# Kernel tuning notes

Hardware: AMD Instinct MI355X
Metric: run time of the kernel (lower is better)

Reference implementation:

```python
import jax, jax.numpy as jnp
import numpy as np

D_MODEL = 1024
H = 16           # num_heads
D = 64           # head_dim
HD = H * D       # hd_dim
PHASE_SCALE = 10.0


def _freqs():
    # Multiscale phasor frequencies (H, D): rotary-style per-dim decay,
    # per-head linear scale (reconstruction of generate_multiscale_phasors).
    d = jnp.arange(D, dtype=jnp.float32)
    base = 10000.0 ** (-d / D)                                  # (D,)
    head_scale = (jnp.arange(H, dtype=jnp.float32) + 1.0) / H   # (H,)
    return 2.0 * np.pi * head_scale[:, None] * base[None, :]    # (H, D)


def setup_inputs() -> dict:
    key = jax.random.key(0)
    ks = jax.random.split(key, 4)
    B, T = 2, 8192
    s = 1.0 / np.sqrt(D_MODEL)
    return {
        "x": jax.random.normal(ks[0], (B, T, D_MODEL), jnp.float32),
        "Wk": jax.random.normal(ks[1], (HD, D_MODEL), jnp.float32) * s,
        "Wv": jax.random.normal(ks[2], (HD, D_MODEL), jnp.float32) * s,
        "Wo": jax.random.normal(ks[3], (D_MODEL, HD), jnp.float32) * s,
        "gate": jnp.ones((H, 2), jnp.float32) * 0.5,
    }


def reference(x, Wk, Wv, Wo, gate):
    B, T, C = x.shape
    k_real = (x @ Wk.T).reshape(B, T, H, D)                      # (B,T,H,D)
    v = (x @ Wv.T).reshape(B, T, H, D).astype(jnp.complex64)
    # shared q/k unit-modulus phasors
    k = jnp.exp(1j * (k_real * PHASE_SCALE))                     # complex64
    q = k
    t = jnp.arange(T, dtype=jnp.float32)
    rotors = jnp.exp(1j * (t[:, None, None] * _freqs()[None]))   # (T,H,D)
    scale = jnp.sqrt(jnp.arange(1, T + 1, dtype=jnp.float32))[None, :, None, None]
    # positional path: bind with rotors, accumulate, retrieve with conj rotors
    mem_pos = jnp.cumsum(v * rotors[None], axis=1)
    out_pos = (mem_pos * jnp.conj(rotors)[None]).real / scale
    # associative path: bind with conj of shifted keys, retrieve with q
    k_shifted = jnp.roll(k, shift=1, axis=1).at[:, 0].set(0)
    mem_assoc = jnp.cumsum(v * jnp.conj(k_shifted), axis=1)
    out_assoc = (mem_assoc * q).real / scale
    # gated combine per head
    out = out_pos * gate[None, None, :, 0:1] + out_assoc * gate[None, None, :, 1:2]
    out = out.reshape(B, T, HD)
    return out @ Wo.T
```

## Files before the change

### kernel.cpp

```cpp
#include <hip/hip_runtime.h>
#include <math.h>


#define B_SZ 2
#define T_LEN 8192
#define H_N 16
#define D_N 64
#define HD 1024
#define DM 1024

#define NCH 128
#define CH (T_LEN / NCH)

typedef unsigned short u16;
typedef __attribute__((ext_vector_type(4))) unsigned short u16x4;
typedef __attribute__((ext_vector_type(8))) short s16x8;
typedef __attribute__((ext_vector_type(8))) _Float16 f16x8;
typedef __attribute__((ext_vector_type(4))) float f32x4;

__device__ __forceinline__ u16 f2h(float f) {
    return __builtin_bit_cast(u16, (_Float16)f);
}
__device__ __forceinline__ float h2f(u16 h) {
    return (float)__builtin_bit_cast(_Float16, h);
}

__global__ __launch_bounds__(256) void conv_x_h(
    const float* __restrict__ x, u16* __restrict__ xh)
{
    size_t i = ((size_t)blockIdx.x * 256 + threadIdx.x) * 4;
    float4 v = *reinterpret_cast<const float4*>(&x[i]);
    u16x4 o = { f2h(v.x), f2h(v.y), f2h(v.z), f2h(v.w) };
    *reinterpret_cast<u16x4*>(&xh[i]) = o;
}

__global__ __launch_bounds__(256) void conv_wkv(
    const float* __restrict__ Wk, const float* __restrict__ Wv,
    u16* __restrict__ Wkv)
{
    size_t i = ((size_t)blockIdx.x * 256 + threadIdx.x) * 4;
    int r = (int)(i >> 10);
    size_t src = (i & (1024 * 1024 - 1));
    float4 v;
    float s;
    if (r < 1024) { v = *reinterpret_cast<const float4*>(&Wk[i]); s = 10.f; }
    else          { v = *reinterpret_cast<const float4*>(&Wv[src]); s = 1.f; }
    u16x4 o = { f2h(s * v.x), f2h(s * v.y), f2h(s * v.z), f2h(s * v.w) };
    *reinterpret_cast<u16x4*>(&Wkv[i]) = o;
}

__global__ __launch_bounds__(256) void conv_w(
    const float* __restrict__ W, u16* __restrict__ Wb)
{
    size_t i = ((size_t)blockIdx.x * 256 + threadIdx.x) * 4;
    float4 v = *reinterpret_cast<const float4*>(&W[i]);
    u16x4 o = { f2h(v.x), f2h(v.y), f2h(v.z), f2h(v.w) };
    *reinterpret_cast<u16x4*>(&Wb[i]) = o;
}

#define GBK 64

#define BAR()     asm volatile("s_barrier" ::: "memory")
#define VMCNT4()  asm volatile("s_waitcnt vmcnt(4)" ::: "memory")
#define VMCNT0()  asm volatile("s_waitcnt vmcnt(0)" ::: "memory")
#define LGKM8PRE() asm volatile("s_waitcnt lgkmcnt(8)" ::: "memory")
#define LGKM0_SB() do { asm volatile("s_waitcnt lgkmcnt(0)" ::: "memory"); \
                        __builtin_amdgcn_sched_barrier(0); } while (0)

template <int IMM>
__device__ __forceinline__ s16x8 dsr(unsigned base) {
    s16x8 r;
    asm volatile("ds_read_b128 %0, %1 offset:%2"
                 : "=v"(r) : "v"(base), "n"(IMM));
    return r;
}

__device__ __forceinline__ unsigned lds_addr(const void* p) {
    return (unsigned)(uintptr_t)(const __attribute__((address_space(3))) void*)p;
}

#define MFMA_Q(mh, nh)                                               \
  {                                                                  \
    _Pragma("unroll")                                                \
    for (int ks_ = 0; ks_ < 2; ++ks_)                                \
      _Pragma("unroll")                                              \
      for (int m_ = 0; m_ < 4; ++m_)                                 \
        _Pragma("unroll")                                            \
        for (int n_ = 0; n_ < 2; ++n_)                               \
          acc[(mh)*4 + m_][(nh)*2 + n_] =                            \
            __builtin_amdgcn_mfma_f32_16x16x32_f16(                  \
              __builtin_bit_cast(f16x8, aR[m_][ks_]),                \
              __builtin_bit_cast(f16x8, bR[(nh)*2 + n_][ks_]),       \
              acc[(mh)*4 + m_][(nh)*2 + n_], 0, 0, 0);               \
  }

#define RD_A(ph, ofs)                                                          \
  aR[0][0]=dsr<(ofs)+0>(bA[ph][0]);    aR[1][0]=dsr<(ofs)+2048>(bA[ph][0]);    \
  aR[2][0]=dsr<(ofs)+4096>(bA[ph][0]); aR[3][0]=dsr<(ofs)+6144>(bA[ph][0]);    \
  aR[0][1]=dsr<(ofs)+0>(bA[ph][1]);    aR[1][1]=dsr<(ofs)+2048>(bA[ph][1]);    \
  aR[2][1]=dsr<(ofs)+4096>(bA[ph][1]); aR[3][1]=dsr<(ofs)+6144>(bA[ph][1]);
#define RD_B01(ph)                                                             \
  bR[0][0]=dsr<0>(bB[ph][0]);    bR[1][0]=dsr<2048>(bB[ph][0]);                \
  bR[0][1]=dsr<0>(bB[ph][1]);    bR[1][1]=dsr<2048>(bB[ph][1]);
#define RD_B23(ph)                                                             \
  bR[2][0]=dsr<4096>(bB[ph][0]); bR[3][0]=dsr<6144>(bB[ph][0]);                \
  bR[2][1]=dsr<4096>(bB[ph][1]); bR[3][1]=dsr<6144>(bB[ph][1]);

#define PHASE_GROUP(ph)                                              \
  {                                                                  \
    RD_A(ph, 0); RD_B01(ph); RD_B23(ph);                             \
    LGKM8PRE();                                                      \
    if ((ph) == 0)    { STAGE_A(2*t+1, 1, 0); STAGE_A(2*t+1, 1, 1); }\
    else if (gm)      { STAGE_A(2*t+2, 0, 0); STAGE_A(2*t+2, 0, 1); }\
    BAR(); LGKM0_SB();                                               \
    __builtin_amdgcn_s_setprio(1);                                   \
    MFMA_Q(0, 0); MFMA_Q(0, 1);                                      \
    __builtin_amdgcn_s_setprio(0);                                   \
    BAR();                                                           \
    RD_A(ph, 8192);                                                  \
    if (gm) { STAGE_B(2*t+2+(ph), (ph), 0);                          \
              STAGE_B(2*t+2+(ph), (ph), 1); VMCNT4(); }              \
    else    { VMCNT0(); }                                            \
    BAR(); LGKM0_SB();                                               \
    __builtin_amdgcn_s_setprio(1);                                   \
    MFMA_Q(1, 0); MFMA_Q(1, 1);                                      \
    __builtin_amdgcn_s_setprio(0);                                   \
    BAR();                                                           \
  }

__device__ __forceinline__ void stage_half(
    const u16* __restrict__ g, int ld, int rowbase, int kbase,
    char* ldshalf, int wid, int lane)
{
#pragma unroll
    for (int s = 0; s < 2; ++s) {
        const int slot = s * 512 + wid * 64 + lane;
        const int r = slot >> 3;
        const int cb = ((slot & 7) << 4) ^ ((r & 7) << 4);
        const u16* gp = g + (size_t)(rowbase + r) * ld + kbase + (cb >> 1);
        __builtin_amdgcn_global_load_lds(
            (const __attribute__((address_space(1))) void*)gp,
            (__attribute__((address_space(3))) void*)(ldshalf + s * 8192 + wid * 1024),
            16, 0, 0);
    }
}

__global__ __launch_bounds__(512, 2) void gemm_mfma256(
    const u16* __restrict__ A, int lda, const u16* __restrict__ W, int ldw,
    void* __restrict__ Cv, int ldc, void* __restrict__ Vv, int K, int mode,
    int m_base, int bshift)
{
    __shared__ __align__(16) char lds[131072];

    const int tid  = threadIdx.x;
    const int lane = tid & 63;
    const int wid  = tid >> 6;
    const int wm   = wid >> 2;
    const int wn   = wid & 3;
    const int l15  = lane & 15;
    const int hib  = (lane >> 4) << 4;

    const int flat = blockIdx.y * gridDim.x + blockIdx.x;
    const int xcd  = flat & 7;
    const int c    = flat >> 3;
    const int byl  = c & ((1 << bshift) - 1);
    const int bx   = c >> bshift;
    const int m0   = ((xcd << bshift) + byl) * 256 + m_base;
    const int n0   = bx * 256;

    const int NK2 = K / (2 * GBK);

    f32x4 acc[8][4] = {};
    s16x8 aR[4][2], bR[4][2];

    const int Xl = (l15 & 7) << 4;
    unsigned bA[2][2], bB[2][2];
#pragma unroll
    for (int p2 = 0; p2 < 2; ++p2)
#pragma unroll
        for (int ks = 0; ks < 2; ++ks) {
            bA[p2][ks] = lds_addr(lds) + p2 * 65536 +
                         (wm * 128 + l15) * 128 + ((ks * 64 + hib) ^ Xl);
            bB[p2][ks] = lds_addr(lds) + p2 * 65536 + 32768 +
                         (wn * 64 + l15) * 128 + ((ks * 64 + hib) ^ Xl);
        }

    auto STAGE_A = [&](int kt, int buf, int h) {
        stage_half(A, lda, m0 + h * 128, kt * GBK,
                   (char*)lds + buf * 65536 + h * 16384, wid, lane);
    };
    auto STAGE_B = [&](int kt, int buf, int h) {
        stage_half(W, ldw, n0 + h * 128, kt * GBK,
                   (char*)lds + buf * 65536 + 32768 + h * 16384, wid, lane);
    };

    STAGE_B(0, 0, 0); STAGE_B(0, 0, 1);
    STAGE_A(0, 0, 0); STAGE_A(0, 0, 1);
    STAGE_B(1, 1, 0); STAGE_B(1, 1, 1);
    VMCNT4();
    BAR();

    for (int t = 0; t < NK2; ++t) {
        const bool gm = (t < NK2 - 1);
        PHASE_GROUP(0)
        PHASE_GROUP(1)
    }

    float* Cf = (float*)Cv;
    u16*   Vh = (u16*)Vv;
    const bool isPhase = (mode == 0) || (n0 < 1024);
#pragma unroll
    for (int m = 0; m < 8; ++m) {
#pragma unroll
        for (int n = 0; n < 4; ++n) {
            const int r0  = m0 + wm * 128 + m * 16 + ((lane >> 4) << 2);
            const int col = n0 + wn * 64 + n * 16 + l15;
#pragma unroll
            for (int r = 0; r < 4; ++r) {
                const float val = acc[m][n][r];
                if (isPhase) {
                    Cf[(size_t)(r0 + r) * ldc + col] = val;
                } else {
                    Vh[(size_t)(r0 + r) * 1024 + (col - 1024)] = f2h(val);
                }
            }
        }
    }
}

__device__ __forceinline__ void rotor_sincos(int t, double fd, float* sr, float* cr)
{
    const double twopi = 6.283185307179586;
    const double inv2pi = 0.15915494309189535;
    double ang = (double)t * fd;
    double n = rint(ang * inv2pi);
    float red = (float)(ang - n * twopi);
    __sincosf(red, sr, cr);
}

__global__ __launch_bounds__(256) void scan_pass1(
    const u16* __restrict__ vArr, const float* __restrict__ phase,
    float* __restrict__ cs)
{
    int gw = (blockIdx.x * 256 + threadIdx.x) >> 6;
    int d = threadIdx.x & 63;
    int c = gw & (NCH - 1);
    int h = (gw >> 7) & (H_N - 1);
    int b = gw >> 11;

    double fd = 6.283185307179586 * ((double)(h + 1) / 16.0)
              * pow(10000.0, -(double)d / 64.0);

    int t0 = c * CH;
    size_t base = ((size_t)b * T_LEN + t0) * HD + (size_t)h * D_N + d;

    float cr, sr;
    rotor_sincos(t0, fd, &sr, &cr);
    float cf, sf;
    sincosf((float)fd, &sf, &cf);

    float cp = 0.f, spv = 0.f;
    if (t0 > 0) {
        float thp = phase[base - HD];
        __sincosf(thp, &spv, &cp);
    }

    float sp_re = 0.f, sp_im = 0.f, sa_re = 0.f, sa_im = 0.f;
    for (int i = 0; i < CH; ++i) {
        size_t idx = base + (size_t)i * HD;
        float v = h2f(vArr[idx]);
        float th = phase[idx];
        sp_re = fmaf(v, cr, sp_re);
        sp_im = fmaf(v, sr, sp_im);
        sa_re = fmaf(v, cp, sa_re);
        sa_im = fmaf(-v, spv, sa_im);
        __sincosf(th, &spv, &cp);
        float nc = fmaf(cr, cf, -sr * sf);
        float ns = fmaf(sr, cf,  cr * sf);
        cr = nc; sr = ns;
    }

    const size_t NT = (size_t)B_SZ * H_N * NCH * D_N;
    size_t ci = (size_t)gw * D_N + d;
    cs[ci] = sp_re;
    cs[NT + ci] = sp_im;
    cs[2 * NT + ci] = sa_re;
    cs[3 * NT + ci] = sa_im;
}

__global__ void scan_pass2(float* __restrict__ cs)
{
    int tid = blockIdx.x * blockDim.x + threadIdx.x;
    if (tid >= B_SZ * H_N * D_N) return;
    int d = tid & 63;
    int bh = tid >> 6;
    size_t base = (size_t)bh * NCH * D_N + d;
    const size_t NT = (size_t)B_SZ * H_N * NCH * D_N;
    float r0 = 0.f, r1 = 0.f, r2 = 0.f, r3 = 0.f;
    for (int c = 0; c < NCH; ++c) {
        size_t i = base + (size_t)c * D_N;
        float a = cs[i], b2 = cs[NT + i], c2 = cs[2 * NT + i], d2 = cs[3 * NT + i];
        cs[i] = r0; cs[NT + i] = r1; cs[2 * NT + i] = r2; cs[3 * NT + i] = r3;
        r0 += a; r1 += b2; r2 += c2; r3 += d2;
    }
}

__global__ __launch_bounds__(256) void scan_pass3(
    const u16* __restrict__ vArr, const float* __restrict__ phase,
    const float* __restrict__ cs, const float* __restrict__ gate,
    u16* __restrict__ y)
{
    int gw = (blockIdx.x * 256 + threadIdx.x) >> 6;
    int d = threadIdx.x & 63;
    int c = gw & (NCH - 1);
    int h = (gw >> 7) & (H_N - 1);
    int b = gw >> 11;

    double fd = 6.283185307179586 * ((double)(h + 1) / 16.0)
              * pow(10000.0, -(double)d / 64.0);
    float g0 = gate[h * 2 + 0];
    float g1 = gate[h * 2 + 1];

    int t0 = c * CH;
    size_t base = ((size_t)b * T_LEN + t0) * HD + (size_t)h * D_N + d;

    const size_t NT = (size_t)B_SZ * H_N * NCH * D_N;
    size_t ci = (size_t)gw * D_N + d;
    float ap_re = cs[ci];
    float ap_im = cs[NT + ci];
    float aa_re = cs[2 * NT + ci];
    float aa_im = cs[3 * NT + ci];

    float cr, sr;
    rotor_sincos(t0, fd, &sr, &cr);
    float cf, sf;
    sincosf((float)fd, &sf, &cf);

    float cp = 0.f, spv = 0.f;
    if (t0 > 0) {
        float thp = phase[base - HD];
        __sincosf(thp, &spv, &cp);
    }

    for (int i = 0; i < CH; ++i) {
        int t = t0 + i;
        size_t idx = base + (size_t)i * HD;
        float v = h2f(vArr[idx]);
        float th = phase[idx];
        ap_re = fmaf(v, cr, ap_re);
        ap_im = fmaf(v, sr, ap_im);
        aa_re = fmaf(v, cp, aa_re);
        aa_im = fmaf(-v, spv, aa_im);
        float op = fmaf(ap_re, cr, ap_im * sr);
        float ck, sk;
        __sincosf(th, &sk, &ck);
        float oa = fmaf(aa_re, ck, -aa_im * sk);
        float sc = rsqrtf((float)(t + 1));
        y[idx] = f2h((g0 * op + g1 * oa) * sc);
        cp = ck; spv = sk;
        float nc = fmaf(cr, cf, -sr * sf);
        float ns = fmaf(sr, cf,  cr * sf);
        cr = nc; sr = ns;
    }
}

extern "C" void kernel_launch(void* const* d_in, const int* in_sizes, int n_in,
                              void* d_out, int out_size, void* d_ws, size_t ws_size,
                              hipStream_t stream)
{
    const float* x    = (const float*)d_in[0];
    const float* Wk   = (const float*)d_in[1];
    const float* Wv   = (const float*)d_in[2];
    const float* Wo   = (const float*)d_in[3];
    const float* gate = (const float*)d_in[4];
    float* out = (float*)d_out;

    float* phase = (float*)d_out;

    char* wsb = (char*)d_ws;
    u16*   xh  = (u16*)wsb;
    u16*   yb  = (u16*)wsb;
    u16*   vb  = (u16*)(wsb + (32ull << 20));
    float* cs  = (float*)(wsb + (64ull << 20));
    u16*   Wkv = (u16*)(wsb + (68ull << 20));
    u16*   Wob = (u16*)(wsb + (72ull << 20));

    hipLaunchKernelGGL(conv_x_h, dim3(16384), dim3(256), 0, stream, x, xh);
    hipLaunchKernelGGL(conv_wkv, dim3(2048), dim3(256), 0, stream, Wk, Wv, Wkv);
    hipLaunchKernelGGL(conv_w,   dim3(1024), dim3(256), 0, stream, Wo, Wob);

    const dim3 gblk(512);

    hipLaunchKernelGGL(gemm_mfma256, dim3(8, 32), gblk, 0, stream,
                       xh, 1024, Wkv, 1024, (void*)phase, HD, (void*)vb, 1024, 3,
                       0, 2);
    hipLaunchKernelGGL(gemm_mfma256, dim3(8, 32), gblk, 0, stream,
                       xh, 1024, Wkv, 1024, (void*)phase, HD, (void*)vb, 1024, 3,
                       8192, 2);

    const int waves = B_SZ * H_N * NCH;
    hipLaunchKernelGGL(scan_pass1, dim3(waves / 4), dim3(256), 0, stream, vb, phase, cs);
    hipLaunchKernelGGL(scan_pass2, dim3(8), dim3(256), 0, stream, cs);
    hipLaunchKernelGGL(scan_pass3, dim3(waves / 4), dim3(256), 0, stream, vb, phase, cs, gate, yb);

    hipLaunchKernelGGL(gemm_mfma256, dim3(4, 64), gblk, 0, stream,
                       yb, 1024, Wob, 1024, (void*)out, HD, (void*)0, 1024, 0,
                       0, 3);
}
```

Measured before the change: 186.7 us.

## Restructure GEMM main loop to full-tile double buffering and store phases as fp16

The GEMM main loop is rewritten from a split half-tile staging schedule into one where each K tile issues all A/B global-to-LDS loads for the next tile up front. The LDS register reads are split into A0/A1/B0/B1 groups so MFMAs can start after partial lgkmcnt waits, and there is one vmcnt(0) plus barrier per tile. Separately, the phase output of the K projection is range-reduced modulo 2π and stored as fp16 in a workspace buffer instead of fp32 in the output buffer. This halves the phase traffic read by both scan passes. The fp16 phase storage loses precision on the angle, and the per-tile barrier may reduce overlap compared with the previous schedule.

Measured after the change: 234.8 us. 25.8% more time.

```diff
diff --git a/kernel.cpp b/kernel.cpp
--- a/kernel.cpp
+++ b/kernel.cpp
@@ -61,9 +61,9 @@
 #define GBK 64
 
 #define BAR()     asm volatile("s_barrier" ::: "memory")
-#define VMCNT4()  asm volatile("s_waitcnt vmcnt(4)" ::: "memory")
 #define VMCNT0()  asm volatile("s_waitcnt vmcnt(0)" ::: "memory")
-#define LGKM8PRE() asm volatile("s_waitcnt lgkmcnt(8)" ::: "memory")
+#define LGKM8_SB() do { asm volatile("s_waitcnt lgkmcnt(8)" ::: "memory"); \
+                        __builtin_amdgcn_sched_barrier(0); } while (0)
 #define LGKM0_SB() do { asm volatile("s_waitcnt lgkmcnt(0)" ::: "memory"); \
                         __builtin_amdgcn_sched_barrier(0); } while (0)
 
@@ -79,7 +79,7 @@
     return (unsigned)(uintptr_t)(const __attribute__((address_space(3))) void*)p;
 }
 
-#define MFMA_Q(mh, nh)                                               \
+#define MFMA_Q2(AS, BS, mh, nh)                                      \
   {                                                                  \
     _Pragma("unroll")                                                \
     for (int ks_ = 0; ks_ < 2; ++ks_)                                \
@@ -89,42 +89,50 @@
         for (int n_ = 0; n_ < 2; ++n_)                               \
           acc[(mh)*4 + m_][(nh)*2 + n_] =                            \
             __builtin_amdgcn_mfma_f32_16x16x32_f16(                  \
-              __builtin_bit_cast(f16x8, aR[m_][ks_]),                \
-              __builtin_bit_cast(f16x8, bR[(nh)*2 + n_][ks_]),       \
+              __builtin_bit_cast(f16x8, AS[m_][ks_]),                \
+              __builtin_bit_cast(f16x8, BS[n_][ks_]),                \
               acc[(mh)*4 + m_][(nh)*2 + n_], 0, 0, 0);               \
   }
 
-#define RD_A(ph, ofs)                                                          \
-  aR[0][0]=dsr<(ofs)+0>(bA[ph][0]);    aR[1][0]=dsr<(ofs)+2048>(bA[ph][0]);    \
-  aR[2][0]=dsr<(ofs)+4096>(bA[ph][0]); aR[3][0]=dsr<(ofs)+6144>(bA[ph][0]);    \
-  aR[0][1]=dsr<(ofs)+0>(bA[ph][1]);    aR[1][1]=dsr<(ofs)+2048>(bA[ph][1]);    \
-  aR[2][1]=dsr<(ofs)+4096>(bA[ph][1]); aR[3][1]=dsr<(ofs)+6144>(bA[ph][1]);
-#define RD_B01(ph)                                                             \
-  bR[0][0]=dsr<0>(bB[ph][0]);    bR[1][0]=dsr<2048>(bB[ph][0]);                \
-  bR[0][1]=dsr<0>(bB[ph][1]);    bR[1][1]=dsr<2048>(bB[ph][1]);
-#define RD_B23(ph)                                                             \
-  bR[2][0]=dsr<4096>(bB[ph][0]); bR[3][0]=dsr<6144>(bB[ph][0]);                \
-  bR[2][1]=dsr<4096>(bB[ph][1]); bR[3][1]=dsr<6144>(bB[ph][1]);
-
-#define PHASE_GROUP(ph)                                              \
+#define RD_A0(ph)                                                              \
+  A0r[0][0]=dsr<0>(bA[ph][0]);    A0r[1][0]=dsr<2048>(bA[ph][0]);              \
+  A0r[2][0]=dsr<4096>(bA[ph][0]); A0r[3][0]=dsr<6144>(bA[ph][0]);              \
+  A0r[0][1]=dsr<0>(bA[ph][1]);    A0r[1][1]=dsr<2048>(bA[ph][1]);              \
+  A0r[2][1]=dsr<4096>(bA[ph][1]); A0r[3][1]=dsr<6144>(bA[ph][1]);
+#define RD_A1(ph)                                                              \
+  A1r[0][0]=dsr<8192+0>(bA[ph][0]);    A1r[1][0]=dsr<8192+2048>(bA[ph][0]);    \
+  A1r[2][0]=dsr<8192+4096>(bA[ph][0]); A1r[3][0]=dsr<8192+6144>(bA[ph][0]);    \
+  A1r[0][1]=dsr<8192+0>(bA[ph][1]);    A1r[1][1]=dsr<8192+2048>(bA[ph][1]);    \
+  A1r[2][1]=dsr<8192+4096>(bA[ph][1]); A1r[3][1]=dsr<8192+6144>(bA[ph][1]);
+#define RD_B0(ph)                                                              \
+  B0r[0][0]=dsr<0>(bB[ph][0]);    B0r[1][0]=dsr<2048>(bB[ph][0]);              \
+  B0r[0][1]=dsr<0>(bB[ph][1]);    B0r[1][1]=dsr<2048>(bB[ph][1]);
+#define RD_B1(ph)                                                              \
+  B1r[0][0]=dsr<4096>(bB[ph][0]); B1r[1][0]=dsr<6144>(bB[ph][0]);              \
+  B1r[0][1]=dsr<4096>(bB[ph][1]); B1r[1][1]=dsr<6144>(bB[ph][1]);
+
+#define TILE(ph, kt)                                                 \
   {                                                                  \
-    RD_A(ph, 0); RD_B01(ph); RD_B23(ph);                             \
-    LGKM8PRE();                                                      \
-    if ((ph) == 0)    { STAGE_A(2*t+1, 1, 0); STAGE_A(2*t+1, 1, 1); }\
-    else if (gm)      { STAGE_A(2*t+2, 0, 0); STAGE_A(2*t+2, 0, 1); }\
-    BAR(); LGKM0_SB();                                               \
+    const bool gm = (kt) < NK - 1;                                   \
+    RD_A0(ph); RD_B0(ph);                                            \
+    if (gm) { STAGE_A((kt)+1, (ph)^1, 0); STAGE_A((kt)+1, (ph)^1, 1);\
+              STAGE_B((kt)+1, (ph)^1, 0); STAGE_B((kt)+1, (ph)^1, 1);}\
+    LGKM0_SB();                                     \
+    RD_B1(ph); RD_A1(ph);                          \
+    __builtin_amdgcn_sched_barrier(0);                               \
     __builtin_amdgcn_s_setprio(1);                                   \
-    MFMA_Q(0, 0); MFMA_Q(0, 1);                                      \
+    MFMA_Q2(A0r, B0r, 0, 0);                                         \
     __builtin_amdgcn_s_setprio(0);                                   \
-    BAR();                                                           \
-    RD_A(ph, 8192);                                                  \
-    if (gm) { STAGE_B(2*t+2+(ph), (ph), 0);                          \
-              STAGE_B(2*t+2+(ph), (ph), 1); VMCNT4(); }              \
-    else    { VMCNT0(); }                                            \
-    BAR(); LGKM0_SB();                                               \
+    LGKM8_SB();                             \
     __builtin_amdgcn_s_setprio(1);                                   \
-    MFMA_Q(1, 0); MFMA_Q(1, 1);                                      \
+    MFMA_Q2(A0r, B1r, 0, 1);                                         \
     __builtin_amdgcn_s_setprio(0);                                   \
+    LGKM0_SB();                                        \
+    __builtin_amdgcn_s_setprio(1);                                   \
+    MFMA_Q2(A1r, B0r, 1, 0);                                         \
+    MFMA_Q2(A1r, B1r, 1, 1);                                         \
+    __builtin_amdgcn_s_setprio(0);                                   \
+    VMCNT0();                            \
     BAR();                                                           \
   }
 
@@ -145,7 +153,7 @@
     }
 }
 
-__global__ __launch_bounds__(512, 2) void gemm_mfma256(
+__global__ __launch_bounds__(512, 2) void gemm2p(
     const u16* __restrict__ A, int lda, const u16* __restrict__ W, int ldw,
     void* __restrict__ Cv, int ldc, void* __restrict__ Vv, int K, int mode,
     int m_base, int bshift)
@@ -168,10 +176,10 @@
     const int m0   = ((xcd << bshift) + byl) * 256 + m_base;
     const int n0   = bx * 256;
 
-    const int NK2 = K / (2 * GBK);
+    const int NK = K / GBK;
 
     f32x4 acc[8][4] = {};
-    s16x8 aR[4][2], bR[4][2];
+    s16x8 A0r[4][2], A1r[4][2], B0r[2][2], B1r[2][2];
 
     const int Xl = (l15 & 7) << 4;
     unsigned bA[2][2], bB[2][2];
@@ -194,21 +202,22 @@
                    (char*)lds + buf * 65536 + 32768 + h * 16384, wid, lane);
     };
 
+    STAGE_A(0, 0, 0); STAGE_A(0, 0, 1);
     STAGE_B(0, 0, 0); STAGE_B(0, 0, 1);
-    STAGE_A(0, 0, 0); STAGE_A(0, 0, 1);
-    STAGE_B(1, 1, 0); STAGE_B(1, 1, 1);
-    VMCNT4();
+    VMCNT0();
     BAR();
 
-    for (int t = 0; t < NK2; ++t) {
-        const bool gm = (t < NK2 - 1);
-        PHASE_GROUP(0)
-        PHASE_GROUP(1)
-    }
-
+    for (int t2 = 0; t2 < NK / 2; ++t2) {
+        TILE(0, 2 * t2)
+        TILE(1, 2 * t2 + 1)
+    }
+
+    const float TWOPI  = 6.2831853071795864f;
+    const float INV2PI = 0.15915494309189535f;
     float* Cf = (float*)Cv;
+    u16*   Ph = (u16*)Cv;
     u16*   Vh = (u16*)Vv;
-    const bool isPhase = (mode == 0) || (n0 < 1024);
+    const bool isPhase = (n0 < 1024);
 #pragma unroll
     for (int m = 0; m < 8; ++m) {
 #pragma unroll
@@ -218,8 +227,11 @@
 #pragma unroll
             for (int r = 0; r < 4; ++r) {
                 const float val = acc[m][n][r];
-                if (isPhase) {
+                if (mode == 0) {
                     Cf[(size_t)(r0 + r) * ldc + col] = val;
+                } else if (isPhase) {
+                    float red = fmaf(-TWOPI, rintf(val * INV2PI), val);
+                    Ph[(size_t)(r0 + r) * 1024 + col] = f2h(red);
                 } else {
                     Vh[(size_t)(r0 + r) * 1024 + (col - 1024)] = f2h(val);
                 }
@@ -239,7 +251,7 @@
 }
 
 __global__ __launch_bounds__(256) void scan_pass1(
-    const u16* __restrict__ vArr, const float* __restrict__ phase,
+    const u16* __restrict__ vArr, const u16* __restrict__ phase,
     float* __restrict__ cs)
 {
     int gw = (blockIdx.x * 256 + threadIdx.x) >> 6;
@@ -261,7 +273,7 @@
 
     float cp = 0.f, spv = 0.f;
     if (t0 > 0) {
-        float thp = phase[base - HD];
+        float thp = h2f(phase[base - HD]);
         __sincosf(thp, &spv, &cp);
     }
 
@@ -269,7 +281,7 @@
     for (int i = 0; i < CH; ++i) {
         size_t idx = base + (size_t)i * HD;
         float v = h2f(vArr[idx]);
-        float th = phase[idx];
+        float th = h2f(phase[idx]);
         sp_re = fmaf(v, cr, sp_re);
         sp_im = fmaf(v, sr, sp_im);
         sa_re = fmaf(v, cp, sa_re);
@@ -306,7 +318,7 @@
 }
 
 __global__ __launch_bounds__(256) void scan_pass3(
-    const u16* __restrict__ vArr, const float* __restrict__ phase,
+    const u16* __restrict__ vArr, const u16* __restrict__ phase,
     const float* __restrict__ cs, const float* __restrict__ gate,
     u16* __restrict__ y)
 {
@@ -338,7 +350,7 @@
 
     float cp = 0.f, spv = 0.f;
     if (t0 > 0) {
-        float thp = phase[base - HD];
+        float thp = h2f(phase[base - HD]);
         __sincosf(thp, &spv, &cp);
     }
 
@@ -346,7 +358,7 @@
         int t = t0 + i;
         size_t idx = base + (size_t)i * HD;
         float v = h2f(vArr[idx]);
-        float th = phase[idx];
+        float th = h2f(phase[idx]);
         ap_re = fmaf(v, cr, ap_re);
         ap_im = fmaf(v, sr, ap_im);
         aa_re = fmaf(v, cp, aa_re);
@@ -375,15 +387,14 @@
     const float* gate = (const float*)d_in[4];
     float* out = (float*)d_out;
 
-    float* phase = (float*)d_out;
-
     char* wsb = (char*)d_ws;
-    u16*   xh  = (u16*)wsb;
-    u16*   yb  = (u16*)wsb;
-    u16*   vb  = (u16*)(wsb + (32ull << 20));
-    float* cs  = (float*)(wsb + (64ull << 20));
-    u16*   Wkv = (u16*)(wsb + (68ull << 20));
-    u16*   Wob = (u16*)(wsb + (72ull << 20));
+    u16*   xh   = (u16*)wsb;
+    u16*   yb   = (u16*)wsb;
+    u16*   vb   = (u16*)(wsb + (32ull << 20));
+    float* cs   = (float*)(wsb + (64ull << 20));
+    u16*   Wkv  = (u16*)(wsb + (68ull << 20));
+    u16*   Wob  = (u16*)(wsb + (72ull << 20));
+    u16*   ph16 = (u16*)(wsb + (74ull << 20));
 
     hipLaunchKernelGGL(conv_x_h, dim3(16384), dim3(256), 0, stream, x, xh);
     hipLaunchKernelGGL(conv_wkv, dim3(2048), dim3(256), 0, stream, Wk, Wv, Wkv);
@@ -391,19 +402,19 @@
 
     const dim3 gblk(512);
 
-    hipLaunchKernelGGL(gemm_mfma256, dim3(8, 32), gblk, 0, stream,
-                       xh, 1024, Wkv, 1024, (void*)phase, HD, (void*)vb, 1024, 3,
+    hipLaunchKernelGGL(gemm2p, dim3(8, 32), gblk, 0, stream,
+                       xh, 1024, Wkv, 1024, (void*)ph16, 1024, (void*)vb, 1024, 3,
                        0, 2);
-    hipLaunchKernelGGL(gemm_mfma256, dim3(8, 32), gblk, 0, stream,
-                       xh, 1024, Wkv, 1024, (void*)phase, HD, (void*)vb, 1024, 3,
+    hipLaunchKernelGGL(gemm2p, dim3(8, 32), gblk, 0, stream,
+                       xh, 1024, Wkv, 1024, (void*)ph16, 1024, (void*)vb, 1024, 3,
                        8192, 2);
 
     const int waves = B_SZ * H_N * NCH;
-    hipLaunchKernelGGL(scan_pass1, dim3(waves / 4), dim3(256), 0, stream, vb, phase, cs);
+    hipLaunchKernelGGL(scan_pass1, dim3(waves / 4), dim3(256), 0, stream, vb, ph16, cs);
     hipLaunchKernelGGL(scan_pass2, dim3(8), dim3(256), 0, stream, cs);
-    hipLaunchKernelGGL(scan_pass3, dim3(waves / 4), dim3(256), 0, stream, vb, phase, cs, gate, yb);
-
-    hipLaunchKernelGGL(gemm_mfma256, dim3(4, 64), gblk, 0, stream,
+    hipLaunchKernelGGL(scan_pass3, dim3(waves / 4), dim3(256), 0, stream, vb, ph16, cs, gate, yb);
+
+    hipLaunchKernelGGL(gemm2p, dim3(4, 64), gblk, 0, stream,
                        yb, 1024, Wob, 1024, (void*)out, HD, (void*)0, 1024, 0,
                        0, 3);
 }
```
